# Optimization experiments

Hardware: AMD Instinct MI355X
Metric: run time of the kernel (lower is better)

The kernel has to match this reference:

```python
import jax, jax.numpy as jnp
import numpy as np

HIDDEN = 4096
N_HEADS = 32
HEAD_DIM = HIDDEN // N_HEADS
B = 8
S = 1024
N = B * S


def _build_cos_sin(max_pos, head_dim):
    inv_freq = 1.0 / (10000.0 ** (np.arange(0, head_dim, 2, dtype=np.float32) / head_dim))
    t = np.arange(max_pos, dtype=np.float32)
    freqs = np.outer(t, inv_freq)                 # [max_pos, head_dim/2]
    emb = np.concatenate([freqs, freqs], axis=-1)  # [max_pos, head_dim]
    return jnp.asarray(np.cos(emb)), jnp.asarray(np.sin(emb))


def setup_inputs() -> dict:
    key = jax.random.key(0)
    ks = jax.random.split(key, 5)
    cos, sin = _build_cos_sin(S, HEAD_DIM)
    scale = 0.02
    inp = {
        "cos": cos,
        "sin": sin,
        "nz_hidden_states": jax.random.normal(ks[0], (N, HIDDEN), jnp.float32),
        "nz_position_ids": jnp.tile(jnp.arange(S, dtype=jnp.int32), B),
        "cu_seqlens": jnp.arange(B + 1, dtype=jnp.int32) * S,
        "max_seqlen": S,
        "Wq": jax.random.normal(ks[1], (HIDDEN, HIDDEN), jnp.float32) * scale,
        "Wk": jax.random.normal(ks[2], (HIDDEN, HIDDEN), jnp.float32) * scale,
        "Wv": jax.random.normal(ks[3], (HIDDEN, HIDDEN), jnp.float32) * scale,
        "Wo": jax.random.normal(ks[4], (HIDDEN, HIDDEN), jnp.float32) * scale,
    }
    return inp


def _rotate_half(x):
    x1, x2 = jnp.split(x, 2, axis=-1)
    return jnp.concatenate([-x2, x1], axis=-1)


def reference(cos, sin, nz_hidden_states, nz_position_ids, cu_seqlens, max_seqlen, Wq, Wk, Wv, Wo):
    n_tok = nz_hidden_states.shape[0]
    b = cu_seqlens.shape[0] - 1
    s = n_tok // b  # equal-length packing
    h, d = N_HEADS, HEAD_DIM

    q = (nz_hidden_states @ Wq.T).reshape(n_tok, h, d)
    k = (nz_hidden_states @ Wk.T).reshape(n_tok, h, d)
    v = (nz_hidden_states @ Wv.T).reshape(n_tok, h, d)

    # RoPE: cos/sin gathered per token, broadcast over heads
    c = cos[nz_position_ids][:, None, :]  # [N,1,D]
    sn = sin[nz_position_ids][:, None, :]
    q = q * c + _rotate_half(q) * sn
    k = k * c + _rotate_half(k) * sn

    # Varlen causal attention (equal-length segments -> batch reshape)
    qb = q.reshape(b, s, h, d)
    kb = k.reshape(b, s, h, d)
    vb = v.reshape(b, s, h, d)
    scores = jnp.einsum('bqhd,bkhd->bhqk', qb, kb) / jnp.sqrt(jnp.float32(d))
    causal = jnp.tril(jnp.ones((s, s), dtype=bool))
    scores = jnp.where(causal, scores, jnp.finfo(scores.dtype).min)
    probs = jax.nn.softmax(scores, axis=-1)
    out = jnp.einsum('bhqk,bkhd->bqhd', probs, vb).reshape(n_tok, h * d)
    return out @ Wo.T
```

## Files before the change

### kernel.cpp

```cpp
#include <hip/hip_runtime.h>
#include <hip/hip_bf16.h>

#define NTOK 8192
#define HID 4096
#define NHEADS 32
#define HDIM 128
#define SEQ 1024
#define NSTEP (HID / 32)

typedef float f32x4 __attribute__((ext_vector_type(4)));
typedef short bf16x8 __attribute__((ext_vector_type(8)));

__device__ __forceinline__ ushort f2bf(float f) {
  union { float f; unsigned u; } x;
  x.f = f;
  unsigned r = x.u + 0x7fffu + ((x.u >> 16) & 1u);
  return (ushort)(r >> 16);
}
__device__ __forceinline__ float bf2f(ushort h) {
  union { unsigned u; float f; } x;
  x.u = ((unsigned)h) << 16;
  return x.f;
}

__global__ __launch_bounds__(256) void cvt_bf16_kernel(const float4* __restrict__ in,
                                                       ushort4* __restrict__ out, int n4) {
  int i = blockIdx.x * 256 + threadIdx.x;
  if (i < n4) {
    float4 v = in[i];
    ushort4 o;
    o.x = f2bf(v.x); o.y = f2bf(v.y); o.z = f2bf(v.z); o.w = f2bf(v.w);
    out[i] = o;
  }
}


__device__ __forceinline__ void gload16(const void* g, void* l) {
  __builtin_amdgcn_global_load_lds(
      (const __attribute__((address_space(1))) unsigned int*)g,
      (__attribute__((address_space(3))) unsigned int*)l, 16, 0, 0);
}

__device__ __forceinline__ void stage32(const ushort* gA, const ushort* gB,
                                        int rowA0, int rowB0, int k0,
                                        ushort* ldsA, ushort* ldsB, int tid) {
  const int wid = tid >> 6, lane = tid & 63;
#pragma unroll
  for (int q = 0; q < 2; ++q) {
    int wuni = q * 8192 + wid * 1024;
    int off = wuni + lane * 16;
    int row = off >> 6;
    int kb = (off ^ (((row >> 1) & 3) << 4)) & 63;
    gload16(gA + (size_t)(rowA0 + row) * HID + k0 + (kb >> 1), (char*)ldsA + wuni);
    gload16(gB + (size_t)(rowB0 + row) * HID + k0 + (kb >> 1), (char*)ldsB + wuni);
  }
}

#define GSTEP(T, DO_STAGE, VMC)                                                \
  do {                                                                         \
    const char* cA = (const char*)ringA[(T) & 3];                              \
    const char* cB = (const char*)ringB[(T) & 3];                              \
    _Pragma("unroll") for (int ii = 0; ii < 8; ++ii) {                         \
      int L = (wm * 128 + ii * 16 + l15) * 64 + l4 * 16;                       \
      af[ii] = *(const bf16x8*)(cA + (L ^ swzr));                              \
    }                                                                          \
    _Pragma("unroll") for (int jj = 0; jj < 4; ++jj) {                         \
      int L = (wn * 64 + jj * 16 + l15) * 64 + l4 * 16;                        \
      bfr[jj] = *(const bf16x8*)(cB + (L ^ swzr));                             \
    }                                                                          \
    if (DO_STAGE)                                                              \
      stage32(Abf, Bp, m0, n0, ((T) + 3) * 32, ringA[((T) + 3) & 3],           \
              ringB[((T) + 3) & 3], tid);                                      \
    _Pragma("unroll") for (int ii = 0; ii < 8; ++ii)                           \
        _Pragma("unroll") for (int jj = 0; jj < 4; ++jj)                       \
            acc[ii][jj] = __builtin_amdgcn_mfma_f32_16x16x32_bf16(             \
                af[ii], bfr[jj], acc[ii][jj], 0, 0, 0);                        \
    if ((VMC) >= 0) {                                                          \
      asm volatile("s_waitcnt lgkmcnt(0)" ::: "memory");                       \
      if ((VMC) == 4) asm volatile("s_waitcnt vmcnt(4)" ::: "memory");         \
      else asm volatile("s_waitcnt vmcnt(0)" ::: "memory");                    \
      __builtin_amdgcn_s_barrier();                                            \
    }                                                                          \
  } while (0)

template <bool OUTF32>
__global__ __launch_bounds__(512, 2) void gemm256_kernel(
    const ushort* __restrict__ Abf,
    const ushort* __restrict__ B0, const ushort* __restrict__ B1,
    const ushort* __restrict__ B2,
    void* __restrict__ O0, void* __restrict__ O1, void* __restrict__ O2,
    int NTALL) {
  __shared__ __align__(16) ushort ringA[4][8192];
  __shared__ __align__(16) ushort ringB[4][8192];

  const int tid = threadIdx.x;
  const int l = tid & 63, wid = tid >> 6;
  const int wm = wid >> 2, wn = wid & 3;
  const int l15 = l & 15, l4 = l >> 4;
  const int swzr = ((l15 >> 1) & 3) << 4;

  const int nwg = gridDim.x;
  const int cpx = nwg >> 3;
  const int bid = blockIdx.x;
  const int lgid = (bid & 7) * cpx + (bid >> 3);
  const int bandw = NTALL << 3;
  const int band = lgid / bandw, rem = lgid % bandw;
  const int nt = rem >> 3;
  const int mt = (band << 3) + (rem & 7);
  const int m0 = mt * 256;
  const int sel = nt >> 4;
  const int n0 = (nt & 15) * 256;
  const ushort* Bp = (sel == 0) ? B0 : ((sel == 1) ? B1 : B2);
  void* Op = (sel == 0) ? O0 : ((sel == 1) ? O1 : O2);

  f32x4 acc[8][4];
  const f32x4 zero = {0.f, 0.f, 0.f, 0.f};
#pragma unroll
  for (int i = 0; i < 8; ++i)
#pragma unroll
    for (int j = 0; j < 4; ++j) acc[i][j] = zero;

  stage32(Abf, Bp, m0, n0, 0, ringA[0], ringB[0], tid);
  stage32(Abf, Bp, m0, n0, 32, ringA[1], ringB[1], tid);
  stage32(Abf, Bp, m0, n0, 64, ringA[2], ringB[2], tid);
  asm volatile("s_waitcnt vmcnt(4)" ::: "memory");
  __builtin_amdgcn_s_barrier();

  bf16x8 af[8], bfr[4];
  for (int tt = 0; tt < NSTEP - 4; tt += 4) {
    GSTEP(tt + 0, true, 4);
    GSTEP(tt + 1, true, 4);
    GSTEP(tt + 2, true, 4);
    GSTEP(tt + 3, true, 4);
  }
  GSTEP(NSTEP - 4, true, 4);
  GSTEP(NSTEP - 3, false, 0);
  GSTEP(NSTEP - 2, false, -1);
  GSTEP(NSTEP - 1, false, -1);

#pragma unroll
  for (int i = 0; i < 8; ++i) {
    const int row = m0 + wm * 128 + i * 16 + l4 * 4;
#pragma unroll
    for (int j = 0; j < 4; ++j) {
      const int col = n0 + wn * 64 + j * 16 + l15;
#pragma unroll
      for (int r = 0; r < 4; ++r) {
        float v = acc[i][j][r];
        if constexpr (OUTF32)
          ((float*)Op)[(size_t)(row + r) * HID + col] = v;
        else
          ((ushort*)Op)[(size_t)(row + r) * HID + col] = f2bf(v);
      }
    }
  }
}

template <bool ISBF>
__device__ __forceinline__ void stage_tile(ushort* lds, const void* gp, int row0, int k0, int tid) {
  if constexpr (ISBF) {
    const ushort* g = (const ushort*)gp;
#pragma unroll
    for (int i = 0; i < 2; ++i) {
      int row = (tid >> 2) + i * 64;
      int gr = tid & 3;
      bf16x8 v = *(const bf16x8*)(g + (size_t)(row0 + row) * HID + k0 + gr * 8);
      int gs = gr ^ ((row >> 1) & 3);
      *(bf16x8*)((char*)lds + row * 64 + gs * 16) = v;
    }
  } else {
    const float* g = (const float*)gp;
    int row = tid >> 1;
    const float* rp = g + (size_t)(row0 + row) * HID + k0;
#pragma unroll
    for (int i = 0; i < 2; ++i) {
      int gr = (tid & 1) * 2 + i;
      float4 a = *(const float4*)(rp + gr * 8);
      float4 b = *(const float4*)(rp + gr * 8 + 4);
      bf16x8 v;
      v[0] = (short)f2bf(a.x); v[1] = (short)f2bf(a.y);
      v[2] = (short)f2bf(a.z); v[3] = (short)f2bf(a.w);
      v[4] = (short)f2bf(b.x); v[5] = (short)f2bf(b.y);
      v[6] = (short)f2bf(b.z); v[7] = (short)f2bf(b.w);
      int gs = gr ^ ((row >> 1) & 3);
      *(bf16x8*)((char*)lds + row * 64 + gs * 16) = v;
    }
  }
}

template <bool ABF, bool BBF, bool OUTF32>
__global__ __launch_bounds__(256) void gemm_bt_kernel(
    const void* __restrict__ Ap,
    const void* __restrict__ B0, const void* __restrict__ B1, const void* __restrict__ B2,
    void* __restrict__ O0, void* __restrict__ O1, void* __restrict__ O2,
    int ntiles_per_w) {
  __shared__ __align__(16) ushort lA[128 * 32];
  __shared__ __align__(16) ushort lB[128 * 32];
  const int tid = threadIdx.x;
  const int l = tid & 63, wid = tid >> 6;
  const int wm = wid >> 1, wn = wid & 1;
  const int l15 = l & 15, l4 = l >> 4;
  const int mt0 = blockIdx.y * 128;
  const int ntile = blockIdx.x;
  const int sel = ntile / ntiles_per_w;
  const int nt0 = (ntile % ntiles_per_w) * 128;
  const void* Bp = (sel == 0) ? B0 : ((sel == 1) ? B1 : B2);
  void* Op = (sel == 0) ? O0 : ((sel == 1) ? O1 : O2);

  const f32x4 zero = {0.f, 0.f, 0.f, 0.f};
  f32x4 acc[4][4];
#pragma unroll
  for (int i = 0; i < 4; ++i)
#pragma unroll
    for (int j = 0; j < 4; ++j) acc[i][j] = zero;

  for (int k0 = 0; k0 < HID; k0 += 32) {
    stage_tile<ABF>(lA, Ap, mt0, k0, tid);
    stage_tile<BBF>(lB, Bp, nt0, k0, tid);
    __syncthreads();
    bf16x8 af[4], bfr[4];
#pragma unroll
    for (int i = 0; i < 4; ++i) {
      int rowa = wm * 64 + i * 16 + l15;
      int ga = l4 ^ ((rowa >> 1) & 3);
      af[i] = *(const bf16x8*)((const char*)lA + rowa * 64 + ga * 16);
      int rowb = wn * 64 + i * 16 + l15;
      int gb = l4 ^ ((rowb >> 1) & 3);
      bfr[i] = *(const bf16x8*)((const char*)lB + rowb * 64 + gb * 16);
    }
#pragma unroll
    for (int i = 0; i < 4; ++i)
#pragma unroll
      for (int j = 0; j < 4; ++j)
        acc[i][j] = __builtin_amdgcn_mfma_f32_16x16x32_bf16(af[i], bfr[j], acc[i][j], 0, 0, 0);
    __syncthreads();
  }

#pragma unroll
  for (int i = 0; i < 4; ++i) {
#pragma unroll
    for (int j = 0; j < 4; ++j) {
      int row = mt0 + wm * 64 + i * 16 + l4 * 4;
      int col = nt0 + wn * 64 + j * 16 + l15;
#pragma unroll
      for (int r = 0; r < 4; ++r) {
        float v = acc[i][j][r];
        if constexpr (OUTF32)
          ((float*)Op)[(size_t)(row + r) * HID + col] = v;
        else
          ((ushort*)Op)[(size_t)(row + r) * HID + col] = f2bf(v);
      }
    }
  }
}

__global__ __launch_bounds__(256) void rope_kernel(
    ushort* __restrict__ q, ushort* __restrict__ k,
    const float* __restrict__ cosT, const float* __restrict__ sinT,
    const int* __restrict__ pos) {
  int idx = blockIdx.x * 256 + threadIdx.x;
  int token = idx >> 8;
  int head = (idx >> 3) & 31;
  int c = idx & 7;
  int p = pos[token];
  size_t base = (size_t)token * HID + head * HDIM + c * 8;
  bf16x8 ql = *(bf16x8*)(q + base);
  bf16x8 qh = *(bf16x8*)(q + base + 64);
  bf16x8 kl = *(bf16x8*)(k + base);
  bf16x8 kh = *(bf16x8*)(k + base + 64);
  float4 c0 = *(const float4*)(cosT + (size_t)p * HDIM + c * 8);
  float4 c1 = *(const float4*)(cosT + (size_t)p * HDIM + c * 8 + 4);
  float4 s0 = *(const float4*)(sinT + (size_t)p * HDIM + c * 8);
  float4 s1 = *(const float4*)(sinT + (size_t)p * HDIM + c * 8 + 4);
  float cs[8] = {c0.x, c0.y, c0.z, c0.w, c1.x, c1.y, c1.z, c1.w};
  float sn[8] = {s0.x, s0.y, s0.z, s0.w, s1.x, s1.y, s1.z, s1.w};
  const float qsc = 0.08838834764831845f;
  bf16x8 qlo, qho, klo, kho;
#pragma unroll
  for (int j = 0; j < 8; ++j) {
    float qlf = bf2f((ushort)ql[j]), qhf = bf2f((ushort)qh[j]);
    float klf = bf2f((ushort)kl[j]), khf = bf2f((ushort)kh[j]);
    qlo[j] = (short)f2bf((qlf * cs[j] - qhf * sn[j]) * qsc);
    qho[j] = (short)f2bf((qhf * cs[j] + qlf * sn[j]) * qsc);
    klo[j] = (short)f2bf(klf * cs[j] - khf * sn[j]);
    kho[j] = (short)f2bf(khf * cs[j] + klf * sn[j]);
  }
  *(bf16x8*)(q + base) = qlo;
  *(bf16x8*)(q + base + 64) = qho;
  *(bf16x8*)(k + base) = klo;
  *(bf16x8*)(k + base + 64) = kho;
}

__global__ __launch_bounds__(512) void attn_kernel(
    const ushort* __restrict__ qb, const ushort* __restrict__ kb,
    const ushort* __restrict__ vb, ushort* __restrict__ ob) {
  __shared__ __align__(16) ushort lK[32 * 128];
  __shared__ __align__(16) ushort lVT[128 * 32];
  __shared__ __align__(16) ushort lP[8][16 * 32];

  const int tid = threadIdx.x;
  const int l = tid & 63, wid = tid >> 6;
  const int l15 = l & 15, l4 = l >> 4;
  const int q0 = (gridDim.x - 1 - blockIdx.x) * 128;
  const int h = blockIdx.y;
  const size_t seqbase = (size_t)blockIdx.z * SEQ;

  const int sr = tid >> 4, sg = tid & 15;
  const int vd = tid & 127, vj0 = (tid >> 7) * 8;
  const ushort* kgp = kb + (seqbase + sr) * HID + h * HDIM + sg * 8;
  const ushort* vgp = vb + (seqbase + vj0) * HID + h * HDIM + vd;

  bf16x8 qf[4];
  {
    const ushort* qp = qb + (seqbase + q0 + wid * 16 + l15) * HID + h * HDIM + l4 * 8;
#pragma unroll
    for (int kk = 0; kk < 4; ++kk) qf[kk] = *(const bf16x8*)(qp + kk * 32);
  }

  const f32x4 zero = {0.f, 0.f, 0.f, 0.f};
  f32x4 oacc[8];
#pragma unroll
  for (int t = 0; t < 8; ++t) oacc[t] = zero;
  float mrow[4] = {-3e38f, -3e38f, -3e38f, -3e38f};
  float lrow[4] = {0.f, 0.f, 0.f, 0.f};

  const int ntile = q0 / 32 + 4;

  bf16x8 kreg = *(const bf16x8*)(kgp);
  bf16x8 vreg;
#pragma unroll
  for (int j = 0; j < 8; ++j) vreg[j] = (short)vgp[(size_t)j * HID];

  for (int kt = 0; kt < ntile; ++kt) {
    const int k0 = kt * 32;
    __builtin_amdgcn_s_barrier();
    {
      int gs = sg ^ (sr & 7);
      *(bf16x8*)((char*)lK + sr * 256 + gs * 16) = kreg;
    }
    {
      int g = tid >> 7;
      int gs = g ^ ((vd >> 1) & 3);
      *(bf16x8*)((char*)lVT + vd * 64 + gs * 16) = vreg;
    }
    if (kt + 1 < ntile) {
      const size_t off = (size_t)(k0 + 32) * HID;
      kreg = *(const bf16x8*)(kgp + off);
#pragma unroll
      for (int j = 0; j < 8; ++j) vreg[j] = (short)vgp[off + (size_t)j * HID];
    }
    __syncthreads();

    f32x4 s[2];
#pragma unroll
    for (int hf = 0; hf < 2; ++hf) {
      f32x4 c = zero;
      int row = hf * 16 + l15;
#pragma unroll
      for (int kk = 0; kk < 4; ++kk) {
        int gs = (kk * 4 + l4) ^ (row & 7);
        bf16x8 kf = *(const bf16x8*)((const char*)lK + row * 256 + gs * 16);
        c = __builtin_amdgcn_mfma_f32_16x16x32_bf16(qf[kk], kf, c, 0, 0, 0);
      }
      s[hf] = c;
    }

    const int qrow = q0 + wid * 16 + l4 * 4;
#pragma unroll
    for (int r = 0; r < 4; ++r) {
      float s0 = (k0 + l15 <= qrow + r) ? s[0][r] : -1e30f;
      float s1 = (k0 + 16 + l15 <= qrow + r) ? s[1][r] : -1e30f;
      float tmax = fmaxf(s0, s1);
#pragma unroll
      for (int off = 8; off; off >>= 1) tmax = fmaxf(tmax, __shfl_xor(tmax, off));
      float newm = fmaxf(mrow[r], tmax);
      float sc = __expf(mrow[r] - newm);
      float p0 = __expf(s0 - newm);
      float p1 = __expf(s1 - newm);
      float rs = p0 + p1;
#pragma unroll
      for (int off = 8; off; off >>= 1) rs += __shfl_xor(rs, off);
      lrow[r] = lrow[r] * sc + rs;
      mrow[r] = newm;
#pragma unroll
      for (int t = 0; t < 8; ++t) oacc[t][r] *= sc;
      lP[wid][(l4 * 4 + r) * 32 + l15] = f2bf(p0);
      lP[wid][(l4 * 4 + r) * 32 + 16 + l15] = f2bf(p1);
    }
    asm volatile("s_waitcnt lgkmcnt(0)" ::: "memory");
    __builtin_amdgcn_sched_barrier(0);

    bf16x8 pf = *(const bf16x8*)((const char*)&lP[wid][0] + l15 * 64 + l4 * 16);
#pragma unroll
    for (int t = 0; t < 8; ++t) {
      int d = t * 16 + l15;
      int gs = l4 ^ ((d >> 1) & 3);
      bf16x8 vf = *(const bf16x8*)((const char*)lVT + d * 64 + gs * 16);
      oacc[t] = __builtin_amdgcn_mfma_f32_16x16x32_bf16(pf, vf, oacc[t], 0, 0, 0);
    }
  }

#pragma unroll
  for (int r = 0; r < 4; ++r) {
    float inv = 1.0f / lrow[r];
    ushort* op = ob + (seqbase + q0 + wid * 16 + l4 * 4 + r) * HID + h * HDIM + l15;
#pragma unroll
    for (int t = 0; t < 8; ++t) op[t * 16] = f2bf(oacc[t][r] * inv);
  }
}

extern "C" void kernel_launch(void* const* d_in, const int* in_sizes, int n_in,
                              void* d_out, int out_size, void* d_ws, size_t ws_size,
                              hipStream_t stream) {
  const float* cosT = (const float*)d_in[0];
  const float* sinT = (const float*)d_in[1];
  const float* X    = (const float*)d_in[2];
  const int*   pos  = (const int*)d_in[3];
  const float* Wq = (const float*)d_in[6];
  const float* Wk = (const float*)d_in[7];
  const float* Wv = (const float*)d_in[8];
  const float* Wo = (const float*)d_in[9];
  float* out = (float*)d_out;

  char* ws = (char*)d_ws;
  const size_t QKVB = (size_t)NTOK * HID * 2;
  const size_t WB = (size_t)HID * HID * 2;
  const size_t XB = QKVB;
  ushort* qbuf = (ushort*)(ws);
  ushort* kbuf = (ushort*)(ws + QKVB);
  ushort* vbuf = (ushort*)(ws + 2 * QKVB);

  dim3 blk(256);
  const int n4x = NTOK * HID / 4;
  const int n4w = HID * HID / 4;

  const bool fast = ws_size >= 3 * QKVB + XB + 4 * WB;
  const bool mid = !fast && ws_size >= 3 * QKVB + 2 * WB &&
                   (size_t)out_size * 4 >= XB + 2 * WB;

  if (fast || mid) {
    ushort *xb, *wqb, *wkb, *wvb, *wob;
    if (fast) {
      xb  = (ushort*)(ws + 3 * QKVB);
      wqb = (ushort*)(ws + 3 * QKVB + XB);
      wkb = (ushort*)(ws + 3 * QKVB + XB + WB);
      wvb = (ushort*)(ws + 3 * QKVB + XB + 2 * WB);
      wob = (ushort*)(ws + 3 * QKVB + XB + 3 * WB);
    } else {
      xb  = (ushort*)d_out;
      wqb = (ushort*)((char*)d_out + XB);
      wkb = (ushort*)((char*)d_out + XB + WB);
      wvb = (ushort*)(ws + 3 * QKVB);
      wob = (ushort*)(ws + 3 * QKVB + WB);
    }
    cvt_bf16_kernel<<<n4x / 256, blk, 0, stream>>>((const float4*)X, (ushort4*)xb, n4x);
    cvt_bf16_kernel<<<n4w / 256, blk, 0, stream>>>((const float4*)Wq, (ushort4*)wqb, n4w);
    cvt_bf16_kernel<<<n4w / 256, blk, 0, stream>>>((const float4*)Wk, (ushort4*)wkb, n4w);
    cvt_bf16_kernel<<<n4w / 256, blk, 0, stream>>>((const float4*)Wv, (ushort4*)wvb, n4w);
    cvt_bf16_kernel<<<n4w / 256, blk, 0, stream>>>((const float4*)Wo, (ushort4*)wob, n4w);
    gemm256_kernel<false><<<dim3(32 * 48), dim3(512), 0, stream>>>(
        xb, wqb, wkb, wvb, qbuf, kbuf, vbuf, 48);
    rope_kernel<<<NTOK * NHEADS * 8 / 256, blk, 0, stream>>>(qbuf, kbuf, cosT, sinT, pos);
    attn_kernel<<<dim3(8, 32, 8), dim3(512), 0, stream>>>(qbuf, kbuf, vbuf, qbuf);
    gemm256_kernel<true><<<dim3(32 * 16), dim3(512), 0, stream>>>(
        qbuf, wob, wob, wob, out, out, out, 16);
  } else {
    gemm_bt_kernel<false, false, false><<<dim3(96, 64), blk, 0, stream>>>(
        X, Wq, Wk, Wv, qbuf, kbuf, vbuf, 32);
    rope_kernel<<<NTOK * NHEADS * 8 / 256, blk, 0, stream>>>(qbuf, kbuf, cosT, sinT, pos);
    attn_kernel<<<dim3(8, 32, 8), dim3(512), 0, stream>>>(qbuf, kbuf, vbuf, qbuf);
    gemm_bt_kernel<true, false, true><<<dim3(32, 64), blk, 0, stream>>>(
        qbuf, Wo, Wo, Wo, out, out, out, 32);
  }
}
```

Before: 1.481 ms.

## Double attention KV tile to 64 and drop register prefetch of K/V

Changes the flash-attention key/value tile from 32 to 64 rows, halving loop iterations and barriers per block. The code now computes four score fragments per tile and uses two PV MFMAs per output column group. LDS layouts and swizzles for K, V-transpose and P are updated to match, with a new XOR swizzle on P stores. The previous register prefetch of the next tile's K/V is removed, so global loads are no longer overlapped with compute. The tile also adds an extra barrier at the end of each iteration and uses more LDS.

After: 1.515 ms. 2.3% more time.

```diff
diff --git a/kernel.cpp b/kernel.cpp
--- a/kernel.cpp
+++ b/kernel.cpp
@@ -291,12 +291,13 @@
   *(bf16x8*)(k + base + 64) = kho;
 }
 
+#define KVB 64
 __global__ __launch_bounds__(512) void attn_kernel(
     const ushort* __restrict__ qb, const ushort* __restrict__ kb,
     const ushort* __restrict__ vb, ushort* __restrict__ ob) {
-  __shared__ __align__(16) ushort lK[32 * 128];
-  __shared__ __align__(16) ushort lVT[128 * 32];
-  __shared__ __align__(16) ushort lP[8][16 * 32];
+  __shared__ __align__(16) ushort lK[KVB * 128];
+  __shared__ __align__(16) ushort lVT[128 * KVB];
+  __shared__ __align__(16) ushort lP[8][16 * KVB];
 
   const int tid = threadIdx.x;
   const int l = tid & 63, wid = tid >> 6;
@@ -305,11 +306,6 @@
   const int h = blockIdx.y;
   const size_t seqbase = (size_t)blockIdx.z * SEQ;
 
-  const int sr = tid >> 4, sg = tid & 15;
-  const int vd = tid & 127, vj0 = (tid >> 7) * 8;
-  const ushort* kgp = kb + (seqbase + sr) * HID + h * HDIM + sg * 8;
-  const ushort* vgp = vb + (seqbase + vj0) * HID + h * HDIM + vd;
-
   bf16x8 qf[4];
   {
     const ushort* qp = qb + (seqbase + q0 + wid * 16 + l15) * HID + h * HDIM + l4 * 8;
@@ -324,36 +320,42 @@
   float mrow[4] = {-3e38f, -3e38f, -3e38f, -3e38f};
   float lrow[4] = {0.f, 0.f, 0.f, 0.f};
 
-  const int ntile = q0 / 32 + 4;
-
-  bf16x8 kreg = *(const bf16x8*)(kgp);
-  bf16x8 vreg;
-#pragma unroll
-  for (int j = 0; j < 8; ++j) vreg[j] = (short)vgp[(size_t)j * HID];
-
+  const int ntile = q0 / KVB + 2;
   for (int kt = 0; kt < ntile; ++kt) {
-    const int k0 = kt * 32;
-    __builtin_amdgcn_s_barrier();
+    const int k0 = kt * KVB;
     {
-      int gs = sg ^ (sr & 7);
-      *(bf16x8*)((char*)lK + sr * 256 + gs * 16) = kreg;
+      int r = tid >> 3;
+      const ushort* kp = kb + (seqbase + k0 + r) * HID + h * HDIM;
+#pragma unroll
+      for (int i = 0; i < 2; ++i) {
+        int g = (tid & 7) * 2 + i;
+        bf16x8 kv = *(const bf16x8*)(kp + g * 8);
+        int gs = g ^ (r & 7);
+        *(bf16x8*)((char*)lK + r * 256 + gs * 16) = kv;
+      }
     }
     {
-      int g = tid >> 7;
-      int gs = g ^ ((vd >> 1) & 3);
-      *(bf16x8*)((char*)lVT + vd * 64 + gs * 16) = vreg;
-    }
-    if (kt + 1 < ntile) {
-      const size_t off = (size_t)(k0 + 32) * HID;
-      kreg = *(const bf16x8*)(kgp + off);
-#pragma unroll
-      for (int j = 0; j < 8; ++j) vreg[j] = (short)vgp[off + (size_t)j * HID];
+      int d = tid & 127;
+      int j0 = (tid >> 7) * 16;
+      const ushort* vp = vb + (seqbase + k0 + j0) * HID + h * HDIM + d;
+      ushort tmp[16];
+#pragma unroll
+      for (int j = 0; j < 16; ++j) tmp[j] = vp[(size_t)j * HID];
+#pragma unroll
+      for (int i = 0; i < 2; ++i) {
+        bf16x8 vv;
+#pragma unroll
+        for (int jj = 0; jj < 8; ++jj) vv[jj] = (short)tmp[i * 8 + jj];
+        int g = (j0 >> 3) + i;
+        int gs = g ^ (d & 7);
+        *(bf16x8*)((char*)lVT + d * 128 + gs * 16) = vv;
+      }
     }
     __syncthreads();
 
-    f32x4 s[2];
-#pragma unroll
-    for (int hf = 0; hf < 2; ++hf) {
+    f32x4 s[4];
+#pragma unroll
+    for (int hf = 0; hf < 4; ++hf) {
       f32x4 c = zero;
       int row = hf * 16 + l15;
 #pragma unroll
@@ -368,36 +370,50 @@
     const int qrow = q0 + wid * 16 + l4 * 4;
 #pragma unroll
     for (int r = 0; r < 4; ++r) {
-      float s0 = (k0 + l15 <= qrow + r) ? s[0][r] : -1e30f;
-      float s1 = (k0 + 16 + l15 <= qrow + r) ? s[1][r] : -1e30f;
-      float tmax = fmaxf(s0, s1);
+      float sv[4];
+#pragma unroll
+      for (int hf = 0; hf < 4; ++hf)
+        sv[hf] = (k0 + hf * 16 + l15 <= qrow + r) ? s[hf][r] : -1e30f;
+      float tmax = fmaxf(fmaxf(sv[0], sv[1]), fmaxf(sv[2], sv[3]));
 #pragma unroll
       for (int off = 8; off; off >>= 1) tmax = fmaxf(tmax, __shfl_xor(tmax, off));
       float newm = fmaxf(mrow[r], tmax);
       float sc = __expf(mrow[r] - newm);
-      float p0 = __expf(s0 - newm);
-      float p1 = __expf(s1 - newm);
-      float rs = p0 + p1;
+      float p[4];
+#pragma unroll
+      for (int hf = 0; hf < 4; ++hf) p[hf] = __expf(sv[hf] - newm);
+      float rs = (p[0] + p[1]) + (p[2] + p[3]);
 #pragma unroll
       for (int off = 8; off; off >>= 1) rs += __shfl_xor(rs, off);
       lrow[r] = lrow[r] * sc + rs;
       mrow[r] = newm;
 #pragma unroll
       for (int t = 0; t < 8; ++t) oacc[t][r] *= sc;
-      lP[wid][(l4 * 4 + r) * 32 + l15] = f2bf(p0);
-      lP[wid][(l4 * 4 + r) * 32 + 16 + l15] = f2bf(p1);
+      int prow = l4 * 4 + r;
+      char* pb = (char*)&lP[wid][0] + prow * 128;
+#pragma unroll
+      for (int hf = 0; hf < 4; ++hf)
+        *(ushort*)(pb + (((hf * 16 + l15) * 2) ^ ((prow & 7) << 4))) = f2bf(p[hf]);
     }
     asm volatile("s_waitcnt lgkmcnt(0)" ::: "memory");
     __builtin_amdgcn_sched_barrier(0);
 
-    bf16x8 pf = *(const bf16x8*)((const char*)&lP[wid][0] + l15 * 64 + l4 * 16);
+    bf16x8 pf[2];
+#pragma unroll
+    for (int h2 = 0; h2 < 2; ++h2)
+      pf[h2] = *(const bf16x8*)((const char*)&lP[wid][0] + l15 * 128 +
+                                (((h2 * 4 + l4) * 16) ^ ((l15 & 7) << 4)));
 #pragma unroll
     for (int t = 0; t < 8; ++t) {
       int d = t * 16 + l15;
-      int gs = l4 ^ ((d >> 1) & 3);
-      bf16x8 vf = *(const bf16x8*)((const char*)lVT + d * 64 + gs * 16);
-      oacc[t] = __builtin_amdgcn_mfma_f32_16x16x32_bf16(pf, vf, oacc[t], 0, 0, 0);
-    }
+#pragma unroll
+      for (int h2 = 0; h2 < 2; ++h2) {
+        int gs = (h2 * 4 + l4) ^ (d & 7);
+        bf16x8 vf = *(const bf16x8*)((const char*)lVT + d * 128 + gs * 16);
+        oacc[t] = __builtin_amdgcn_mfma_f32_16x16x32_bf16(pf[h2], vf, oacc[t], 0, 0, 0);
+      }
+    }
+    __syncthreads();
   }
 
 #pragma unroll
```
